# Kernel tuning notes

Hardware: AMD Instinct MI355X
Metric: run time of the kernel (lower is better)

## Reference

```python
import jax, jax.numpy as jnp
import numpy as np

SCALING = 16.0 / 8.0  # lora_alpha / r


def setup_inputs() -> dict:
    key = jax.random.key(0)
    k1, k2, k3, k4 = jax.random.split(key, 4)
    B, S, D_IN, D_OUT, R = 4, 4096, 4096, 4096, 8
    x = jax.random.normal(k1, (B, S, D_IN), dtype=jnp.float32)
    weight = jax.random.normal(k2, (D_OUT, D_IN), dtype=jnp.float32) * 0.02
    lora_A = jax.random.normal(k3, (R, D_IN), dtype=jnp.float32) * 0.02
    lora_B = jax.random.normal(k4, (D_OUT, R), dtype=jnp.float32) * 0.02
    return {"x": x, "weight": weight, "lora_A": lora_A, "lora_B": lora_B}


def reference(x, weight, lora_A, lora_B):
    # Base frozen linear: x @ W^T   (bias='none')
    base = jnp.einsum('bsd,od->bso', x, weight)
    # LoRA path (dropout in eval mode = identity):
    # down-project to rank r, up-project to out, scale, residual-add.
    lora_low = jnp.einsum('bsd,rd->bsr', x, lora_A)      # [B,S,r]
    lora_out = jnp.einsum('bsr,or->bso', lora_low, lora_B)  # [B,S,out]
    return base + lora_out * SCALING
```

## Files before the change

kernel.cpp:

```cpp
#include <hip/hip_runtime.h>
#include <hip/hip_bf16.h>


typedef __bf16 bf16;
typedef bf16 bf16x8 __attribute__((ext_vector_type(8)));
typedef float f32x4 __attribute__((ext_vector_type(4)));

typedef __attribute__((address_space(1))) const void* as1cv;
typedef __attribute__((address_space(3))) void* as3v;

constexpr int Mdim = 16384;
constexpr int Ndim = 4096;
constexpr int Kdim = 4096;
constexpr int Rdim = 8;
constexpr float kScale = 2.0f;

__device__ __forceinline__ unsigned short f2bf(float f) {
  union { float f; unsigned u; } v; v.f = f;
  unsigned u = v.u;
  u += 0x7fffu + ((u >> 16) & 1u);
  return (unsigned short)(u >> 16);
}

__global__ void cast_x_kernel(const float4* __restrict__ x4,
                              ushort4* __restrict__ o4, int n4) {
  int i = blockIdx.x * blockDim.x + threadIdx.x;
  int stride = gridDim.x * blockDim.x;
  for (; i < n4; i += stride) {
    float4 v = x4[i];
    ushort4 o;
    o.x = f2bf(v.x); o.y = f2bf(v.y); o.z = f2bf(v.z); o.w = f2bf(v.w);
    o4[i] = o;
  }
}

__global__ void make_weff_kernel(const float* __restrict__ W,
                                 const float* __restrict__ A,
                                 const float* __restrict__ Bm,
                                 ushort* __restrict__ weff) {
  int tid = blockIdx.x * blockDim.x + threadIdx.x;
  int kc = tid & 511;
  int n = tid >> 9;
  if (n >= Ndim) return;

  const float* wp = W + (long)n * Kdim + kc * 8;
  float4 w0 = *(const float4*)(wp);
  float4 w1 = *(const float4*)(wp + 4);

  float4 b0 = *(const float4*)(Bm + n * Rdim);
  float4 b1 = *(const float4*)(Bm + n * Rdim + 4);
  float bs[8] = {b0.x, b0.y, b0.z, b0.w, b1.x, b1.y, b1.z, b1.w};

  float l[8] = {0.f, 0.f, 0.f, 0.f, 0.f, 0.f, 0.f, 0.f};
#pragma unroll
  for (int r = 0; r < Rdim; ++r) {
    const float* ap = A + (long)r * Kdim + kc * 8;
    float4 a0 = *(const float4*)(ap);
    float4 a1 = *(const float4*)(ap + 4);
    l[0] += bs[r] * a0.x; l[1] += bs[r] * a0.y;
    l[2] += bs[r] * a0.z; l[3] += bs[r] * a0.w;
    l[4] += bs[r] * a1.x; l[5] += bs[r] * a1.y;
    l[6] += bs[r] * a1.z; l[7] += bs[r] * a1.w;
  }

  float o[8] = {w0.x + kScale * l[0], w0.y + kScale * l[1],
                w0.z + kScale * l[2], w0.w + kScale * l[3],
                w1.x + kScale * l[4], w1.y + kScale * l[5],
                w1.z + kScale * l[6], w1.w + kScale * l[7]};
  uint4 pk;
  pk.x = (unsigned)f2bf(o[0]) | ((unsigned)f2bf(o[1]) << 16);
  pk.y = (unsigned)f2bf(o[2]) | ((unsigned)f2bf(o[3]) << 16);
  pk.z = (unsigned)f2bf(o[4]) | ((unsigned)f2bf(o[5]) << 16);
  pk.w = (unsigned)f2bf(o[6]) | ((unsigned)f2bf(o[7]) << 16);
  *(uint4*)(weff + (long)n * Kdim + kc * 8) = pk;
}

#define BM 256
#define BN 256
#define BK 64
#define NT (Kdim / BK)

#define SCHED0 __builtin_amdgcn_sched_barrier(0)
#define BAR __builtin_amdgcn_s_barrier()
#define VMCNT(n) asm volatile("s_waitcnt vmcnt(" #n ")" ::: "memory")
#define LGKM(n) do { asm volatile("s_waitcnt lgkmcnt(" #n ")" ::: "memory"); SCHED0; } while (0)
#define GLOAD(src, dst) \
  __builtin_amdgcn_global_load_lds((as1cv)(src), (as3v)(dst), 16, 0, 0)


__global__ __launch_bounds__(512, 2) void gemm256(const bf16* __restrict__ Xb,
                                                  const bf16* __restrict__ Wb,
                                                  float* __restrict__ C) {
  __shared__ bf16 lds[2][2][2][128 * 64];

  const int tid = threadIdx.x;
  const int lane = tid & 63;
  const int wave = tid >> 6;
  const int wr = wave >> 2;
  const int wc = wave & 3;
  const int fr = lane & 15;
  const int fq = lane >> 4;

  const int wg = blockIdx.x;
  const int swz = (wg & 7) * 128 + (wg >> 3);
  const int by = swz >> 4;
  const int bx = swz & 15;
  const int brow = by * BM;
  const int bcol = bx * BN;

  const int sLow = tid >> 3;
  const int cg = (tid & 7) ^ (sLow & 7);
  const bf16* pA = Xb + (long)(brow + sLow) * Kdim + cg * 8;
  const bf16* pB =
      Wb + (long)(bcol + (sLow & 31) + (sLow >> 5) * 64) * Kdim + cg * 8;

#define STAGE_A(buf, h, kt) do {                                              \
    const bf16* s_ = pA + (long)((h) * 64) * Kdim + (((kt) & (NT - 1)) * 64); \
    GLOAD(s_, &lds[buf][0][h][0] + tid * 8);                                  \
    GLOAD(s_ + (long)128 * Kdim, &lds[buf][0][h][4096] + tid * 8);            \
  } while (0)
#define STAGE_B(buf, h, kt) do {                                              \
    const bf16* s_ = pB + (long)((h) * 32) * Kdim + (((kt) & (NT - 1)) * 64); \
    GLOAD(s_, &lds[buf][1][h][0] + tid * 8);                                  \
    GLOAD(s_ + (long)128 * Kdim, &lds[buf][1][h][4096] + tid * 8);            \
  } while (0)

  const bf16* aBs[2] = {&lds[0][0][0][(wr * 64 + fr) * 64],
                        &lds[1][0][0][(wr * 64 + fr) * 64]};
  const bf16* bBs[2] = {&lds[0][1][0][(wc * 32 + fr) * 64],
                        &lds[1][1][0][(wc * 32 + fr) * 64]};
  const int cofs0 = ((fq + 0) ^ (fr & 7)) * 8;
  const int cofs1 = ((fq + 4) ^ (fr & 7)) * 8;

  f32x4 acc[8][4];
#pragma unroll
  for (int m = 0; m < 8; ++m)
#pragma unroll
    for (int n = 0; n < 4; ++n)
      acc[m][n] = (f32x4){0.f, 0.f, 0.f, 0.f};

  bf16x8 aF0[4][2];
  bf16x8 aF1[4][2];
  bf16x8 bF[2][2][2];

#define LDA(dst, buf, mh)                                                     \
  { _Pragma("unroll") for (int m4 = 0; m4 < 4; ++m4) {                        \
      dst[m4][0] = *(const bf16x8*)(aBs[buf] + (mh) * 8192 + m4 * 1024 + cofs0); \
      dst[m4][1] = *(const bf16x8*)(aBs[buf] + (mh) * 8192 + m4 * 1024 + cofs1); \
  } }
#define LDB(buf, nh)                                                          \
  { _Pragma("unroll") for (int n2 = 0; n2 < 2; ++n2) {                        \
      bF[nh][n2][0] = *(const bf16x8*)(bBs[buf] + (nh) * 8192 + n2 * 1024 + cofs0); \
      bF[nh][n2][1] = *(const bf16x8*)(bBs[buf] + (nh) * 8192 + n2 * 1024 + cofs1); \
  } }
#define MFMAQ(areg, mh, nh)                                                   \
  { __builtin_amdgcn_s_setprio(1);                                            \
    _Pragma("unroll") for (int m4 = 0; m4 < 4; ++m4)                          \
    _Pragma("unroll") for (int n2 = 0; n2 < 2; ++n2)                          \
    _Pragma("unroll") for (int kk = 0; kk < 2; ++kk)                          \
      acc[(mh) * 4 + m4][(nh) * 2 + n2] =                                     \
          __builtin_amdgcn_mfma_f32_16x16x32_bf16(                            \
              areg[m4][kk], bF[nh][n2][kk], acc[(mh) * 4 + m4][(nh) * 2 + n2],\
              0, 0, 0);                                                       \
    __builtin_amdgcn_s_setprio(0); }

#define TILE(bc, bn, t) do {                                                  \
                                                                      \
    STAGE_A(bn, 1, (t) + 1);                                                  \
    LDB(bc, 1);                                                               \
    LGKM(4);                                                                  \
    MFMAQ(aF0, 0, 0);                                                         \
    BAR;                                                                      \
                                                                      \
    STAGE_A(bc, 0, (t) + 2);                                                  \
    LDA(aF1, bc, 1);                                                          \
    LGKM(8);                                                                  \
    MFMAQ(aF0, 0, 1);                                                         \
    BAR;                                                                      \
                                                                      \
    STAGE_B(bc, 0, (t) + 2);                                                  \
    LGKM(0);                                                                  \
    MFMAQ(aF1, 1, 0);                                                         \
    VMCNT(6);                                                                 \
    BAR;                                                                      \
                                                                      \
    LDA(aF0, bn, 0);                                                          \
    LDB(bn, 0);                                                               \
    MFMAQ(aF1, 1, 1);                                                         \
    STAGE_B(bc, 1, (t) + 2);                                                  \
    VMCNT(6);                                                                 \
    BAR;                                                                      \
  } while (0)

  STAGE_A(0, 0, 0); STAGE_B(0, 0, 0); STAGE_B(0, 1, 0); STAGE_A(0, 1, 0);
  STAGE_A(1, 0, 1); STAGE_B(1, 0, 1); STAGE_B(1, 1, 1);
  VMCNT(6); BAR;
  LDA(aF0, 0, 0);
  LDB(0, 0);

#pragma unroll 1
  for (int t = 0; t < NT; t += 2) {
    TILE(0, 1, t);
    TILE(1, 0, t + 1);
  }
  VMCNT(0);
  LGKM(0);

  const int crow = brow + wr * 128 + fq * 4;
  const int ccol = bcol + wc * 64 + fr;
#pragma unroll
  for (int m = 0; m < 8; ++m) {
#pragma unroll
    for (int n = 0; n < 4; ++n) {
      f32x4 v = acc[m][n];
      long base = (long)(crow + m * 16) * Ndim + (ccol + n * 16);
      C[base] = v[0];
      C[base + Ndim] = v[1];
      C[base + 2 * (long)Ndim] = v[2];
      C[base + 3 * (long)Ndim] = v[3];
    }
  }
}

extern "C" void kernel_launch(void* const* d_in, const int* in_sizes, int n_in,
                              void* d_out, int out_size, void* d_ws,
                              size_t ws_size, hipStream_t stream) {
  const float* x = (const float*)d_in[0];
  const float* W = (const float*)d_in[1];
  const float* lA = (const float*)d_in[2];
  const float* lB = (const float*)d_in[3];
  float* out = (float*)d_out;

  ushort* xb = (ushort*)d_ws;
  ushort* weff = xb + (size_t)Mdim * Kdim;

  cast_x_kernel<<<2048, 256, 0, stream>>>((const float4*)x, (ushort4*)xb,
                                          (Mdim * Kdim) / 4);
  make_weff_kernel<<<(Ndim * (Kdim / 8)) / 256, 256, 0, stream>>>(W, lA, lB,
                                                                  weff);
  dim3 grid((Mdim / BM) * (Ndim / BN));
  gemm256<<<grid, 512, 0, stream>>>((const bf16*)xb, (const bf16*)weff, out);
}
```

Measured before the change: 561.2 us.

## Load B fragments directly from global to registers, halve LDS footprint

Drops LDS staging for the weight (B) tile and has each wave load its B MFMA fragments straight from global memory into registers, so LDS holds only the A tiles. The block swizzle is also changed so consecutive workgroups walk along M for a fixed column of W, which should keep the directly read W rows hot in cache. This removes B LDS traffic and frees shared memory, but B is no longer shared across the waves of a row, so global/L2 traffic for W rises and latency is hidden only by the vmcnt waits. The pipeline's wait counts and barriers are reworked to match.

```diff
diff --git a/kernel.cpp b/kernel.cpp
--- a/kernel.cpp
+++ b/kernel.cpp
@@ -82,7 +82,7 @@
 
 #define SCHED0 __builtin_amdgcn_sched_barrier(0)
 #define BAR __builtin_amdgcn_s_barrier()
-#define VMCNT(n) asm volatile("s_waitcnt vmcnt(" #n ")" ::: "memory")
+#define VMCNT(n) do { asm volatile("s_waitcnt vmcnt(" #n ")" ::: "memory"); SCHED0; } while (0)
 #define LGKM(n) do { asm volatile("s_waitcnt lgkmcnt(" #n ")" ::: "memory"); SCHED0; } while (0)
 #define GLOAD(src, dst) \
   __builtin_amdgcn_global_load_lds((as1cv)(src), (as3v)(dst), 16, 0, 0)
@@ -91,7 +91,7 @@
 __global__ __launch_bounds__(512, 2) void gemm256(const bf16* __restrict__ Xb,
                                                   const bf16* __restrict__ Wb,
                                                   float* __restrict__ C) {
-  __shared__ bf16 lds[2][2][2][128 * 64];
+  __shared__ bf16 lds[2][2][128 * 64];
 
   const int tid = threadIdx.x;
   const int lane = tid & 63;
@@ -103,34 +103,27 @@
 
   const int wg = blockIdx.x;
   const int swz = (wg & 7) * 128 + (wg >> 3);
-  const int by = swz >> 4;
-  const int bx = swz & 15;
+  const int bx = swz >> 6;
+  const int by = swz & 63;
   const int brow = by * BM;
   const int bcol = bx * BN;
 
   const int sLow = tid >> 3;
   const int cg = (tid & 7) ^ (sLow & 7);
   const bf16* pA = Xb + (long)(brow + sLow) * Kdim + cg * 8;
-  const bf16* pB =
-      Wb + (long)(bcol + (sLow & 31) + (sLow >> 5) * 64) * Kdim + cg * 8;
 
 #define STAGE_A(buf, h, kt) do {                                              \
     const bf16* s_ = pA + (long)((h) * 64) * Kdim + (((kt) & (NT - 1)) * 64); \
-    GLOAD(s_, &lds[buf][0][h][0] + tid * 8);                                  \
-    GLOAD(s_ + (long)128 * Kdim, &lds[buf][0][h][4096] + tid * 8);            \
+    GLOAD(s_, &lds[buf][h][0] + tid * 8);                                     \
+    GLOAD(s_ + (long)128 * Kdim, &lds[buf][h][4096] + tid * 8);               \
   } while (0)
-#define STAGE_B(buf, h, kt) do {                                              \
-    const bf16* s_ = pB + (long)((h) * 32) * Kdim + (((kt) & (NT - 1)) * 64); \
-    GLOAD(s_, &lds[buf][1][h][0] + tid * 8);                                  \
-    GLOAD(s_ + (long)128 * Kdim, &lds[buf][1][h][4096] + tid * 8);            \
-  } while (0)
-
-  const bf16* aBs[2] = {&lds[0][0][0][(wr * 64 + fr) * 64],
-                        &lds[1][0][0][(wr * 64 + fr) * 64]};
-  const bf16* bBs[2] = {&lds[0][1][0][(wc * 32 + fr) * 64],
-                        &lds[1][1][0][(wc * 32 + fr) * 64]};
+
+  const bf16* aBs[2] = {&lds[0][0][(wr * 64 + fr) * 64],
+                        &lds[1][0][(wr * 64 + fr) * 64]};
   const int cofs0 = ((fq + 0) ^ (fr & 7)) * 8;
   const int cofs1 = ((fq + 4) ^ (fr & 7)) * 8;
+
+  const bf16* pBg = Wb + (long)(bcol + wc * 64 + fr) * Kdim + fq * 8;
 
   f32x4 acc[8][4];
 #pragma unroll
@@ -148,11 +141,11 @@
       dst[m4][0] = *(const bf16x8*)(aBs[buf] + (mh) * 8192 + m4 * 1024 + cofs0); \
       dst[m4][1] = *(const bf16x8*)(aBs[buf] + (mh) * 8192 + m4 * 1024 + cofs1); \
   } }
-#define LDB(buf, nh)                                                          \
-  { _Pragma("unroll") for (int n2 = 0; n2 < 2; ++n2) {                        \
-      bF[nh][n2][0] = *(const bf16x8*)(bBs[buf] + (nh) * 8192 + n2 * 1024 + cofs0); \
-      bF[nh][n2][1] = *(const bf16x8*)(bBs[buf] + (nh) * 8192 + n2 * 1024 + cofs1); \
-  } }
+#define LDBG(nh, kt)                                                          \
+  { _Pragma("unroll") for (int n2 = 0; n2 < 2; ++n2)                          \
+    _Pragma("unroll") for (int kk = 0; kk < 2; ++kk)                          \
+      bF[nh][n2][kk] = *(const bf16x8*)(pBg + (long)((nh) * 32 + n2 * 16) * Kdim \
+                                        + (((kt) & (NT - 1)) * 64 + kk * 32)); }
 #define MFMAQ(areg, mh, nh)                                                   \
   { __builtin_amdgcn_s_setprio(1);                                            \
     _Pragma("unroll") for (int m4 = 0; m4 < 4; ++m4)                          \
@@ -166,37 +159,36 @@
 
 #define TILE(bc, bn, t) do {                                                  \
                                                                       \
+    LDBG(1, t);                                                               \
     STAGE_A(bn, 1, (t) + 1);                                                  \
-    LDB(bc, 1);                                                               \
-    LGKM(4);                                                                  \
+    LGKM(0);                                                                  \
+    VMCNT(6);                                                                 \
     MFMAQ(aF0, 0, 0);                                                         \
-    BAR;                                                                      \
+    SCHED0; BAR;                                                              \
                                                                       \
     STAGE_A(bc, 0, (t) + 2);                                                  \
     LDA(aF1, bc, 1);                                                          \
+    VMCNT(4);                                                                 \
+    MFMAQ(aF0, 0, 1);                                                         \
+    SCHED0; BAR;                                                              \
+                                                                      \
+    LDA(aF0, bn, 0);                                                          \
     LGKM(8);                                                                  \
-    MFMAQ(aF0, 0, 1);                                                         \
-    BAR;                                                                      \
-                                                                      \
-    STAGE_B(bc, 0, (t) + 2);                                                  \
-    LGKM(0);                                                                  \
     MFMAQ(aF1, 1, 0);                                                         \
-    VMCNT(6);                                                                 \
-    BAR;                                                                      \
-                                                                      \
-    LDA(aF0, bn, 0);                                                          \
-    LDB(bn, 0);                                                               \
+    SCHED0; BAR;                                                              \
+                                                                      \
+    LDBG(0, (t) + 1);                                                         \
     MFMAQ(aF1, 1, 1);                                                         \
-    STAGE_B(bc, 1, (t) + 2);                                                  \
-    VMCNT(6);                                                                 \
-    BAR;                                                                      \
+    SCHED0; BAR;                                                              \
   } while (0)
 
-  STAGE_A(0, 0, 0); STAGE_B(0, 0, 0); STAGE_B(0, 1, 0); STAGE_A(0, 1, 0);
-  STAGE_A(1, 0, 1); STAGE_B(1, 0, 1); STAGE_B(1, 1, 1);
-  VMCNT(6); BAR;
+  STAGE_A(0, 0, 0);
+  STAGE_A(0, 1, 0);
+  STAGE_A(1, 0, 1);
+  LDBG(0, 0);
+  VMCNT(8);
+  BAR;
   LDA(aF0, 0, 0);
-  LDB(0, 0);
 
 #pragma unroll 1
   for (int t = 0; t < NT; t += 2) {
```

Measured after the change: 924.9 us. +64.8%, slower.
